# Kernel optimization log

Measured on AMD Instinct MI355X. Metric: run time of the kernel, lower is better.

## Reference

```python
import jax, jax.numpy as jnp
import numpy as np

# ---- DNC configuration (mirrors access_config / controller_config / args) ----
T, B, IN, OUT = 64, 32, 64, 64          # time, batch, input_size, output_size
N, Wd, R, NW = 128, 64, 4, 1            # memory_size, word_size, num_reads, num_writes
H = 256                                  # controller hidden_size (2 LSTM layers)
CLIP = 20.0
EPS = 1e-6
NUM_MODES = 2 * NW + 1                   # backward modes, forward modes, content mode
IF_SIZES = [R*Wd, R, NW*Wd, NW, NW*Wd, NW*Wd, R, NW, NW, R*NUM_MODES]
IF_SIZE = int(np.sum(IF_SIZES))


def setup_inputs() -> dict:
    key = jax.random.key(0)
    ks = jax.random.split(key, 12)
    in0 = IN + R * Wd  # controller input = external input + flattened prev reads

    def w(k, shape, fan):
        return jax.random.normal(k, shape, jnp.float32) / np.float32(np.sqrt(fan))

    return {
        "inputs": jax.random.normal(ks[0], (T, B, IN), jnp.float32),
        "Wx0": w(ks[1], (in0, 4 * H), in0),
        "Wh0": w(ks[2], (H, 4 * H), H),
        "b0": jnp.zeros((4 * H,), jnp.float32),
        "Wx1": w(ks[3], (H, 4 * H), H),
        "Wh1": w(ks[4], (H, 4 * H), H),
        "b1": jnp.zeros((4 * H,), jnp.float32),
        "W_if": w(ks[5], (H, IF_SIZE), H),
        "b_if": jnp.zeros((IF_SIZE,), jnp.float32),
        "W_out": w(ks[6], (H + R * Wd, OUT), H + R * Wd),
        "b_out": jnp.zeros((OUT,), jnp.float32),
    }


def _lstm(x, h, c, Wx, Wh, b):
    g = x @ Wx + h @ Wh + b
    i, f, gg, o = jnp.split(g, 4, axis=-1)
    c2 = jax.nn.sigmoid(f) * c + jax.nn.sigmoid(i) * jnp.tanh(gg)
    h2 = jax.nn.sigmoid(o) * jnp.tanh(c2)
    return h2, c2


def _content_weights(memory, keys, strengths):
    # memory [B,N,W], keys [B,h,W], strengths [B,h] -> [B,h,N]
    mnorm = jnp.linalg.norm(memory, axis=-1)          # [B,N]
    knorm = jnp.linalg.norm(keys, axis=-1)            # [B,h]
    dot = jnp.einsum('bhw,bnw->bhn', keys, memory)
    sim = dot / (knorm[..., None] * mnorm[:, None, :] + EPS)
    return jax.nn.softmax(sim * strengths[..., None], axis=-1)


def _allocation(usage):
    # usage [B,N] -> allocation weighting [B,N] (DNC freeness-based)
    usage = EPS + (1.0 - EPS) * usage
    order = jnp.argsort(usage, axis=-1)               # ascending usage (most free first)
    sorted_usage = jnp.take_along_axis(usage, order, axis=-1)
    prod = jnp.cumprod(sorted_usage, axis=-1)
    prod_excl = jnp.concatenate([jnp.ones_like(prod[:, :1]), prod[:, :-1]], axis=-1)
    alloc_sorted = (1.0 - sorted_usage) * prod_excl
    inv = jnp.argsort(order, axis=-1)
    return jnp.take_along_axis(alloc_sorted, inv, axis=-1)


def _dnc_forward(inputs, Wx0, Wh0, b0, Wx1, Wh1, b1, W_if, b_if, W_out, b_out):
    eye = 1.0 - jnp.eye(N, dtype=jnp.float32)
    splits = np.cumsum(IF_SIZES)[:-1]

    def step(state, x_t):
        h0, c0, h1, c1, M, rw, ww, link, prec, usage, reads = state
        ctrl_in = jnp.concatenate([x_t, reads.reshape(B, R * Wd)], axis=-1)
        h0, c0 = _lstm(ctrl_in, h0, c0, Wx0, Wh0, b0)
        h1, c1 = _lstm(h0, h1, c1, Wx1, Wh1, b1)
        ctrl = jnp.clip(h1, -CLIP, CLIP)

        p = jnp.split(ctrl @ W_if + b_if, splits, axis=-1)
        read_keys = p[0].reshape(B, R, Wd)
        read_str = 1.0 + jax.nn.softplus(p[1])              # oneplus
        write_keys = p[2].reshape(B, NW, Wd)
        write_str = 1.0 + jax.nn.softplus(p[3])
        erase = jax.nn.sigmoid(p[4]).reshape(B, NW, Wd)
        write_vec = p[5].reshape(B, NW, Wd)
        free_g = jax.nn.sigmoid(p[6])                       # [B,R]
        alloc_g = jax.nn.sigmoid(p[7])                      # [B,NW]
        write_g = jax.nn.sigmoid(p[8])                      # [B,NW]
        modes = jax.nn.softmax(p[9].reshape(B, R, NUM_MODES), axis=-1)

        # -- usage update (prev write weights, then free gates on prev reads) --
        cw = 1.0 - jnp.prod(1.0 - ww, axis=1)               # [B,N]
        u = usage + (1.0 - usage) * cw
        psi = jnp.prod(1.0 - free_g[..., None] * rw, axis=1)
        usage = u * psi

        # -- write weights: content + allocation, gated --
        wc = _content_weights(M, write_keys, write_str)     # [B,NW,N]
        u_tmp = usage
        ww_heads = []
        for i in range(NW):
            a = _allocation(u_tmp)
            wg = write_g[:, i:i+1]
            ag = alloc_g[:, i:i+1]
            ww_heads.append(wg * (ag * a + (1.0 - ag) * wc[:, i]))
            u_tmp = u_tmp + (1.0 - u_tmp) * wg * a
        ww = jnp.stack(ww_heads, axis=1)                    # [B,NW,N]

        # -- erase + write memory --
        erase_m = jnp.prod(1.0 - ww[..., None] * erase[:, :, None, :], axis=1)  # [B,N,W]
        add_m = jnp.einsum('bwn,bwk->bnk', ww, write_vec)
        M = M * erase_m + add_m

        # -- temporal link matrix + precedence --
        wi = ww[..., :, None]
        wj = ww[..., None, :]
        link = ((1.0 - wi - wj) * link + wi * prec[..., None, :]) * eye
        prec = (1.0 - ww.sum(axis=-1, keepdims=True)) * prec + ww

        # -- read weights: backward / content / forward modes --
        rc = _content_weights(M, read_keys, read_str)       # [B,R,N]
        fwd = jnp.einsum('bwij,brj->brwi', link, rw)
        bwd = jnp.einsum('bwji,brj->brwi', link, rw)
        bmode = modes[..., :NW]
        fmode = modes[..., NW:2*NW]
        cmode = modes[..., 2*NW]
        rw = (jnp.einsum('brw,brwn->brn', bmode, bwd)
              + cmode[..., None] * rc
              + jnp.einsum('brw,brwn->brn', fmode, fwd))
        reads = jnp.einsum('brn,bnk->brk', rw, M)           # [B,R,W]

        out = jnp.clip(jnp.concatenate([ctrl, reads.reshape(B, R * Wd)], axis=-1) @ W_out + b_out,
                       -CLIP, CLIP)
        return (h0, c0, h1, c1, M, rw, ww, link, prec, usage, reads), out

    z = jnp.zeros
    init = (z((B, H)), z((B, H)), z((B, H)), z((B, H)),
            z((B, N, Wd)), z((B, R, N)), z((B, NW, N)),
            z((B, NW, N, N)), z((B, NW, N)), z((B, N)), z((B, R, Wd)))
    _, outs = jax.lax.scan(step, init, inputs)
    return outs                                            # [T,B,OUT]


def reference(inputs, Wx0, Wh0, b0, Wx1, Wh1, b1, W_if, b_if, W_out, b_out):
    return _dnc_forward(inputs, Wx0, Wh0, b0, Wx1, Wh1, b1, W_if, b_if, W_out, b_out)
```

## Files before the change

kernel.cpp:

```cpp
#include <hip/hip_runtime.h>
#include <math.h>


#define TT   64
#define BB   32
#define INW  64
#define OUTW 64
#define NN   128
#define WD   64
#define RR   4
#define HH   256
#define IFSZ 471
#define CLIPV 20.0f
#define EPSV  1e-6f
#define NBLK 96

#define OFF_RK   0
#define OFF_RSTR 256
#define OFF_WK   260
#define OFF_WSTR 324
#define OFF_ER   325
#define OFF_WV   389
#define OFF_FG   453
#define OFF_AG   457
#define OFF_WG   458
#define OFF_MD   459

#define S_WSTR 0
#define S_AG   1
#define S_WG   2
#define S_KNW  3
#define S_RSTR 8
#define S_FG   12
#define S_KNR  16
#define S_BM   20
#define S_FM   24
#define S_CM   28

#define A_XS   0
#define A_GL   11840
#define A_C0   12896
#define A_GO   13152
#define A_WS   13216
#define A_WO   34528
#define B_XS   0
#define B_GL   9472
#define B_C1   10528
#define B_W1   10784
#define C_MS   0
#define C_LS   8320
#define C_WW   24832
#define C_PRC  24960
#define C_USG  25088
#define C_RWS  25216
#define C_IFC  25728
#define C_FWD  26208
#define C_BWD  26720
#define C_U2   27232
#define C_WCS  27360
#define C_RCS  27488
#define C_MNO  28000
#define C_ERS  28384
#define C_WVS  28448
#define C_SC   28512
#define C_SCAL 28576
#define C_PART2 28608

#define SMEM_FLOATS 36064
#define SMEM_BYTES  (SMEM_FLOATS*4)

#define W_CTL  0
#define W_RDS  8192
#define W_H0   16384
#define W_H1   32768
#define W_FLA  49152
#define W_FLB  (W_FLA + 1024)
#define W_FLC  (W_FLB + 1024)
#define W_END  (W_FLC + 1024)

__device__ __forceinline__ float sigf(float x){ return 1.0f/(1.0f+expf(-x)); }
__device__ __forceinline__ float sofp(float x){ return fmaxf(x,0.0f)+log1pf(expf(-fabsf(x))); }

__device__ __forceinline__ float gload(const float* p){
  return __hip_atomic_load(p, __ATOMIC_RELAXED, __HIP_MEMORY_SCOPE_AGENT);
}
__device__ __forceinline__ void gstore(float* p, float v){
  __hip_atomic_store(p, v, __ATOMIC_RELAXED, __HIP_MEMORY_SCOPE_AGENT);
}
__device__ __forceinline__ void gload8(const float* p, float* a, float* b){
  union { unsigned long long u; float f[2]; } w;
  w.u = __hip_atomic_load((const unsigned long long*)p,
                          __ATOMIC_RELAXED, __HIP_MEMORY_SCOPE_AGENT);
  *a = w.f[0]; *b = w.f[1];
}
__device__ __forceinline__ void gstore8(float* p, float a, float b){
  union { unsigned long long u; float f[2]; } w;
  w.f[0]=a; w.f[1]=b;
  __hip_atomic_store((unsigned long long*)p, w.u,
                     __ATOMIC_RELAXED, __HIP_MEMORY_SCOPE_AGENT);
}

__device__ __forceinline__ void waitflag(const unsigned* slots, unsigned target){
  if (threadIdx.x < 64){
    for (;;){
      unsigned m = __hip_atomic_load(&slots[(threadIdx.x & 31)*32],
                                     __ATOMIC_RELAXED, __HIP_MEMORY_SCOPE_AGENT);
      #pragma unroll
      for (int s=32;s>0;s>>=1){
        unsigned o = (unsigned)__shfl_xor((int)m, s, 64);
        m = (o < m) ? o : m;
      }
      if (m >= target) break;
      __builtin_amdgcn_s_sleep(2);
    }
  }
  __syncthreads();
}

__device__ __forceinline__ void setflag(unsigned* slots, int g, unsigned val){
  asm volatile("s_waitcnt vmcnt(0)" ::: "memory");
  __syncthreads();
  if (threadIdx.x == 0)
    __hip_atomic_store(&slots[g*32], val, __ATOMIC_RELAXED, __HIP_MEMORY_SCOPE_AGENT);
}

__device__ __forceinline__ float wredSum(float v){
  #pragma unroll
  for (int m=32;m>0;m>>=1) v += __shfl_xor(v,m,64);
  return v;
}
__device__ __forceinline__ float wredMax(float v){
  #pragma unroll
  for (int m=32;m>0;m>>=1) v = fmaxf(v,__shfl_xor(v,m,64));
  return v;
}

__device__ __forceinline__ float bfly64(float (&A)[64], int l, int* jb){
  #pragma unroll
  for (int st=0; st<6; ++st){
    const int m = 1<<st, half = 32>>st;
    const bool hi = (l & m) != 0;
    #pragma unroll
    for (int j=0;j<half;j++){
      float a = A[j], b = A[j+half];
      float keep = hi? b : a;
      float send = hi? a : b;
      A[j] = keep + __shfl_xor(send, m, 64);
    }
  }
  *jb = ((l&1)?32:0)|((l&2)?16:0)|((l&4)?8:0)|((l&8)?4:0)|((l&16)?2:0)|((l&32)?1:0);
  return A[0];
}

#define TILE_FMA(WBASE, WROW, XROW)                                      \
  {                                                                      \
    float xv[8], wv[8];                                                  \
    _Pragma("unroll")                                                    \
    for (int q=0;q<8;q++){                                               \
      wv[q] = sm[(WBASE) + (WROW)*37 + c0 + q];                          \
      xv[q] = Xs[(XROW)*37 + b0 + q];                                    \
    }                                                                    \
    _Pragma("unroll")                                                    \
    for (int bi=0;bi<8;bi++)                                             \
      _Pragma("unroll")                                                  \
      for (int ci=0;ci<8;ci++)                                           \
        acc[bi*8+ci] += xv[bi]*wv[ci];                                   \
  }

extern "C" __global__ __launch_bounds__(1024, 1)
void dnc_coop13(const float* __restrict__ inputs,
                const float* __restrict__ Wx0, const float* __restrict__ Wh0, const float* __restrict__ b0g,
                const float* __restrict__ Wx1, const float* __restrict__ Wh1, const float* __restrict__ b1g,
                const float* __restrict__ Wifg, const float* __restrict__ bifg,
                const float* __restrict__ Woutg, const float* __restrict__ boutg,
                float* __restrict__ outg, float* __restrict__ ws)
{
  const int bid  = blockIdx.x;
  const int role = bid >> 5;
  const int g    = bid & 31;
  const int tid  = threadIdx.x;
  const int lane = tid & 63;
  const int wid  = tid >> 6;

  extern __shared__ float sm[];

  float* gctl  = ws + W_CTL;
  float* greads= ws + W_RDS;
  unsigned* fA = (unsigned*)(ws + W_FLA);
  unsigned* fB = (unsigned*)(ws + W_FLB);
  unsigned* fC = (unsigned*)(ws + W_FLC);

  if (role == 0){
    for (int i = tid; i < 576*32; i += 1024){
      int r = i >> 5, cl = i & 31;
      int cglob = 8*g + (cl&7) + ((cl>>3)<<8);
      float v;
      if (r < 256)      v = Wx0[(64+r)*1024 + cglob];
      else if (r < 320) v = Wx0[(r-256)*1024 + cglob];
      else              v = Wh0[(r-320)*1024 + cglob];
      sm[A_WS + r*37 + cl] = v;
    }
    for (int i = tid; i < 512*2; i += 1024){
      int k = i >> 1, c = i & 1;
      sm[A_WO + k*3 + c] = Woutg[k*64 + 2*g + c];
    }
    if (tid < 256) sm[A_C0 + tid] = 0.0f;
  } else if (role == 1){
    for (int i = tid; i < 512*32; i += 1024){
      int r = i >> 5, cl = i & 31;
      int cglob = 8*g + (cl&7) + ((cl>>3)<<8);
      sm[B_W1 + r*37 + cl] = (r < 256) ? Wx1[r*1024 + cglob]
                                       : Wh1[(r-256)*1024 + cglob];
    }
    if (tid < 256) sm[B_C1 + tid] = 0.0f;
  } else {
    for (int i = tid; i < NN*65;  i += 1024) sm[C_MS + i] = 0.0f;
    for (int i = tid; i < NN*129; i += 1024) sm[C_LS + i] = 0.0f;
    if (tid < 128){ sm[C_WW+tid]=0.f; sm[C_PRC+tid]=0.f; sm[C_USG+tid]=0.f; }
    if (tid < 512) sm[C_RWS+tid]=0.f;
  }
  __syncthreads();

  if (role == 0){
    float* Xs = sm + A_XS;
    for (int t = 0; t <= TT; ++t){
      float* h0old = ws + W_H0 + (t&1)*8192;
      float* h0new = ws + W_H0 + ((t+1)&1)*8192;
      float acc[64]; float accO[16];

      waitflag(fA, (unsigned)t);
      if (t < TT){
        for (int i = tid; i < 256*16; i += 1024){
          int k = i>>4, b2 = (i&15)*2;
          float x0,x1; gload8(&h0old[k*32+b2], &x0,&x1);
          Xs[k*37+b2]=x0; Xs[k*37+b2+1]=x1;
        }
        for (int i = tid; i < 64*32; i += 1024){
          int bb = i>>6, k = i&63;
          Xs[(256+k)*37+bb] = inputs[(t*BB + bb)*INW + k];
        }
        __syncthreads();
        #pragma unroll
        for (int j=0;j<64;j++) acc[j]=0.f;
        {
          const int b0 = (wid>>2)*8, c0 = (wid&3)*8;
          #pragma unroll
          for (int i=0;i<4;i++){
            int k = i*64 + lane;
            TILE_FMA(A_WS, 320+k, k)
          }
          TILE_FMA(A_WS, 256+lane, 256+lane)
        }
        __syncthreads();
      }
      if (t > 0){
        waitflag(fB, (unsigned)t);
        for (int i = tid; i < 256*16; i += 1024){
          int k = i>>4, b2 = (i&15)*2;
          float x0,x1; gload8(&gctl[k*32+b2], &x0,&x1);
          Xs[k*37+b2]=x0; Xs[k*37+b2+1]=x1;
        }
        __syncthreads();
        #pragma unroll
        for (int j=0;j<16;j++) accO[j]=0.f;
        if (wid < 4){
          const int b0 = wid*8;
          #pragma unroll
          for (int i=0;i<4;i++){
            int k = i*64 + lane;
            float w0 = sm[A_WO + k*3], w1 = sm[A_WO + k*3 + 1];
            float xv[8];
            #pragma unroll
            for (int q=0;q<8;q++) xv[q] = Xs[k*37 + b0 + q];
            #pragma unroll
            for (int bi=0;bi<8;bi++){
              accO[bi*2]   += xv[bi]*w0;
              accO[bi*2+1] += xv[bi]*w1;
            }
          }
        }
        __syncthreads();
      }
      waitflag(fC, (unsigned)t);
      for (int i = tid; i < 32*128; i += 1024){
        int b = i>>7, k2 = (i&127)*2;
        float x0,x1; gload8(&greads[b*256+k2], &x0,&x1);
        Xs[k2*37+b]=x0; Xs[(k2+1)*37+b]=x1;
      }
      __syncthreads();
      if (t < TT){
        {
          const int b0 = (wid>>2)*8, c0 = (wid&3)*8;
          #pragma unroll
          for (int i=0;i<4;i++){
            int k = i*64 + lane;
            TILE_FMA(A_WS, k, k)
          }
          int jb; float v = bfly64(acc, lane, &jb);
          sm[A_GL + (b0 + (jb>>3))*33 + c0 + (jb&7)] = v;
        }
        __syncthreads();
        if (tid < 128){
          int t2 = tid*2, j = t2>>5, bb = t2&31;
          float hv[2];
          #pragma unroll
          for (int q=0;q<2;q++){
            int b_ = bb+q;
            float gi = sm[A_GL + b_*33 + j]      + b0g[8*g + j];
            float gf = sm[A_GL + b_*33 + 8 + j]  + b0g[256 + 8*g + j];
            float gg = sm[A_GL + b_*33 + 16 + j] + b0g[512 + 8*g + j];
            float go = sm[A_GL + b_*33 + 24 + j] + b0g[768 + 8*g + j];
            float c = sigf(gf)*sm[A_C0 + j*32 + b_] + sigf(gi)*tanhf(gg);
            sm[A_C0 + j*32 + b_] = c;
            hv[q] = sigf(go)*tanhf(c);
          }
          gstore8(&h0new[256*g + t2], hv[0], hv[1]);
        }
        setflag(fA, g, (unsigned)(t+1));
      }
      if (t > 0){
        if (wid < 4){
          const int b0 = wid*8;
          #pragma unroll
          for (int i=0;i<4;i++){
            int k = i*64 + lane;
            float w0 = sm[A_WO + (256+k)*3], w1 = sm[A_WO + (256+k)*3 + 1];
            float xv[8];
            #pragma unroll
            for (int q=0;q<8;q++) xv[q] = Xs[k*37 + b0 + q];
            #pragma unroll
            for (int bi=0;bi<8;bi++){
              accO[bi*2]   += xv[bi]*w0;
              accO[bi*2+1] += xv[bi]*w1;
            }
          }
          #pragma unroll
          for (int st=0; st<4; ++st){
            const int m = 1<<st, half = 8>>st;
            const bool hi = (lane & m) != 0;
            #pragma unroll
            for (int j=0;j<half;j++){
              float a = accO[j], b = accO[j+half];
              float keep = hi? b : a;
              float send = hi? a : b;
              accO[j] = keep + __shfl_xor(send, m, 64);
            }
          }
          accO[0] += __shfl_xor(accO[0], 16, 64);
          accO[0] += __shfl_xor(accO[0], 32, 64);
          int jb = ((lane&1)?8:0)|((lane&2)?4:0)|((lane&4)?2:0)|((lane&8)?1:0);
          if ((lane & 48) == 0){
            int bi = jb>>1, ci = jb&1;
            sm[A_GO + (wid*8+bi)*2 + ci] = accO[0];
          }
        }
        __syncthreads();
        if (tid < 64){
          int bb = tid>>1, c = tid&1;
          float v = sm[A_GO + tid] + boutg[2*g + c];
          outg[((t-1)*BB + bb)*OUTW + 2*g + c] = fminf(CLIPV, fmaxf(-CLIPV, v));
        }
      }
    }
  } else if (role == 1){
    float* Xs = sm + B_XS;
    for (int t = 0; t < TT; ++t){
      float* h0new = ws + W_H0 + ((t+1)&1)*8192;
      float* h1old = ws + W_H1 + (t&1)*8192;
      float* h1new = ws + W_H1 + ((t+1)&1)*8192;
      float acc[64];
      #pragma unroll
      for (int j=0;j<64;j++) acc[j]=0.f;

      waitflag(fB, (unsigned)t);
      for (int i = tid; i < 256*16; i += 1024){
        int k = i>>4, b2 = (i&15)*2;
        float x0,x1; gload8(&h1old[k*32+b2], &x0,&x1);
        Xs[k*37+b2]=x0; Xs[k*37+b2+1]=x1;
      }
      __syncthreads();
      {
        const int b0 = (wid>>2)*8, c0 = (wid&3)*8;
        #pragma unroll
        for (int i=0;i<4;i++){
          int k = i*64 + lane;
          TILE_FMA(B_W1, 256+k, k)
        }
      }
      __syncthreads();
      waitflag(fA, (unsigned)(t+1));
      for (int i = tid; i < 256*16; i += 1024){
        int k = i>>4, b2 = (i&15)*2;
        float x0,x1; gload8(&h0new[k*32+b2], &x0,&x1);
        Xs[k*37+b2]=x0; Xs[k*37+b2+1]=x1;
      }
      __syncthreads();
      {
        const int b0 = (wid>>2)*8, c0 = (wid&3)*8;
        #pragma unroll
        for (int i=0;i<4;i++){
          int k = i*64 + lane;
          TILE_FMA(B_W1, k, k)
        }
        int jb; float v = bfly64(acc, lane, &jb);
        sm[B_GL + (b0 + (jb>>3))*33 + c0 + (jb&7)] = v;
      }
      __syncthreads();
      if (tid < 128){
        int t2 = tid*2, j = t2>>5, bb = t2&31;
        float hv[2], cl2[2];
        #pragma unroll
        for (int q=0;q<2;q++){
          int b_ = bb+q;
          float gi = sm[B_GL + b_*33 + j]      + b1g[8*g + j];
          float gf = sm[B_GL + b_*33 + 8 + j]  + b1g[256 + 8*g + j];
          float gg = sm[B_GL + b_*33 + 16 + j] + b1g[512 + 8*g + j];
          float go = sm[B_GL + b_*33 + 24 + j] + b1g[768 + 8*g + j];
          float c = sigf(gf)*sm[B_C1 + j*32 + b_] + sigf(gi)*tanhf(gg);
          sm[B_C1 + j*32 + b_] = c;
          float h = sigf(go)*tanhf(c);
          hv[q] = h;
          cl2[q] = fminf(CLIPV, fmaxf(-CLIPV, h));
        }
        gstore8(&h1new[256*g + t2], hv[0], hv[1]);
        gstore8(&gctl[256*g + t2], cl2[0], cl2[1]);
      }
      setflag(fB, g, (unsigned)(t+1));
    }
  } else {
    float* Ms  = sm + C_MS;
    float* Ls  = sm + C_LS;
    float* wws = sm + C_WW;
    float* prc = sm + C_PRC;
    float* usg = sm + C_USG;
    float* rws = sm + C_RWS;
    float* ifcl= sm + C_IFC;
    float* fwds= sm + C_FWD;
    float* bwds= sm + C_BWD;
    float* u2  = sm + C_U2;
    float* wcs = sm + C_WCS;
    float* rcs = sm + C_RCS;
    float* mno = sm + C_MNO;
    float* ers = sm + C_ERS;
    float* wvs = sm + C_WVS;
    float* sc  = sm + C_SC;
    float* scal= sm + C_SCAL;
    float* ctl_l = sm + C_RCS;
    float* part2 = sm + C_PART2;

    for (int t = 0; t < TT; ++t){
      if (tid < 128){
        float s=0.f;
        #pragma unroll 8
        for (int d=0;d<WD;d++){ float v=Ms[tid*65+d]; s+=v*v; }
        mno[tid]=sqrtf(s);
      }
      waitflag(fB, (unsigned)(t+1));
      if (tid < 256) ctl_l[tid] = gload(&gctl[tid*32 + g]);
      __syncthreads();
      {
        const int kq = tid >> 8, c = tid & 255;
        const int c2 = c + 256;
        const bool has2 = (c2 < IFSZ);
        const float* Wp = Wifg + (size_t)(kq*64)*IFSZ;
        const float* xp = ctl_l + kq*64;
        float a0=0.f, a1=0.f;
        #pragma unroll 8
        for (int k=0;k<64;k++){
          float x = xp[k];
          a0 += x * Wp[(size_t)k*IFSZ + c];
          if (has2) a1 += x * Wp[(size_t)k*IFSZ + c2];
        }
        part2[kq*512 + c] = a0;
        if (has2) part2[kq*512 + c2] = a1;
      }
      __syncthreads();
      if (tid < IFSZ)
        ifcl[tid] = part2[tid] + part2[512+tid] + part2[1024+tid] + part2[1536+tid] + bifg[tid];
      __syncthreads();

      if (tid < RR){
        scal[S_RSTR+tid]=1.0f+sofp(ifcl[OFF_RSTR+tid]);
        scal[S_FG+tid]  =sigf(ifcl[OFF_FG+tid]);
        float m0=ifcl[OFF_MD+tid*3], m1=ifcl[OFF_MD+tid*3+1], m2=ifcl[OFF_MD+tid*3+2];
        float mx=fmaxf(m0,fmaxf(m1,m2));
        float e0=expf(m0-mx), e1=expf(m1-mx), e2=expf(m2-mx);
        float s=e0+e1+e2;
        scal[S_BM+tid]=e0/s; scal[S_FM+tid]=e1/s; scal[S_CM+tid]=e2/s;
      }
      if (tid == 4) scal[S_WSTR]=1.0f+sofp(ifcl[OFF_WSTR]);
      if (tid == 5) scal[S_AG]=sigf(ifcl[OFF_AG]);
      if (tid == 6) scal[S_WG]=sigf(ifcl[OFF_WG]);
      if (tid >= 64 && tid < 128){
        int d=tid-64;
        ers[d]=sigf(ifcl[OFF_ER+d]);
        wvs[d]=ifcl[OFF_WV+d];
      }
      if (wid == 8){
        float v=ifcl[OFF_WK+lane]; float s=wredSum(v*v);
        if (lane==0) scal[S_KNW]=sqrtf(s);
      }
      if (wid >= 10 && wid < 14){
        int r=wid-10; float v=ifcl[OFF_RK+r*WD+lane]; float s=wredSum(v*v);
        if (lane==0) scal[S_KNR+r]=sqrtf(s);
      }
      __syncthreads();

      if (tid < NN){
        float dot=0.f;
        #pragma unroll 8
        for (int d=0;d<WD;d++) dot += ifcl[OFF_WK+d]*Ms[tid*65+d];
        wcs[tid] = dot/(scal[S_KNW]*mno[tid]+EPSV)*scal[S_WSTR];
      } else if (tid < 256){
        int n = tid-128;
        float cw = wws[n];
        float u  = usg[n] + (1.0f-usg[n])*cw;
        float psi=1.0f;
        #pragma unroll
        for (int r=0;r<RR;r++) psi *= 1.0f - scal[S_FG+r]*rws[r*NN+n];
        float us = u*psi;
        usg[n]=us;
        u2[n] = EPSV + (1.0f-EPSV)*us;
      }
      __syncthreads();
      if (tid < NN){ float mx=wredMax(wcs[tid]); if(lane==0) sc[wid]=mx; }
      __syncthreads();
      if (tid < NN){
        float mx=fmaxf(sc[0],sc[1]);
        float e=expf(wcs[tid]-mx);
        wcs[tid]=e;
        float s=wredSum(e); if(lane==0) sc[2+wid]=s;
      }
      __syncthreads();
      if (tid < 256){
        int n = tid & 127, h = tid >> 7;
        float ui = u2[n]; float p = 1.0f;
        int j0 = h*64;
        for (int j=j0; j<j0+64; j++){
          float uj = u2[j];
          bool take = (uj<ui) || (uj==ui && j<n);
          p *= take ? uj : 1.0f;
        }
        part2[h*128 + n] = p;
      }
      __syncthreads();
      if (tid < NN){
        float wcsum = sc[2]+sc[3];
        float ui=u2[tid];
        float p = part2[tid]*part2[128+tid];
        float a = (1.0f-ui)*p;
        float wwn = scal[S_WG]*( scal[S_AG]*a + (1.0f-scal[S_AG])*(wcs[tid]/wcsum) );
        wws[tid]=wwn;
        float s=wredSum(wwn); if(lane==0) sc[4+wid]=s;
      }
      __syncthreads();
      #pragma unroll
      for (int i=0;i<8;i++){
        int el=tid+i*1024, n=el>>6, d=el&63;
        float w=wws[n];
        Ms[n*65+d] = Ms[n*65+d]*(1.0f - w*ers[d]) + w*wvs[d];
      }
      #pragma unroll
      for (int i=0;i<16;i++){
        int el=tid+i*1024, li=el>>7, lj=el&127;
        float v = (li==lj) ? 0.0f
                : (1.0f - wws[li] - wws[lj])*Ls[li*129+lj] + wws[li]*prc[lj];
        Ls[li*129+lj]=v;
      }
      __syncthreads();
      if (tid < 512){
        int r=tid>>7, n=tid&127;
        float dot=0.f, q=0.f;
        #pragma unroll 8
        for (int d=0;d<WD;d++){
          float m = Ms[n*65+d];
          dot += ifcl[OFF_RK+r*WD+d]*m;
          q   += m*m;
        }
        rcs[tid] = dot/(scal[S_KNR+r]*sqrtf(q)+EPSV)*scal[S_RSTR+r];
      } else {
        int idx=tid-512, r=idx>>7, i=idx&127;
        float f=0.f, bw=0.f;
        const float* rwr = rws + r*NN;
        #pragma unroll 4
        for (int j=0;j<NN;j++){
          float rv=rwr[j];
          f  += Ls[i*129+j]*rv;
          bw += Ls[j*129+i]*rv;
        }
        fwds[idx]=f; bwds[idx]=bw;
      }
      __syncthreads();
      if (tid < 512){ float mx=wredMax(rcs[tid]); if(lane==0) sc[8+wid]=mx; }
      __syncthreads();
      if (tid < 512){
        int r=tid>>7;
        float mx=fmaxf(sc[8+r*2],sc[9+r*2]);
        float e=expf(rcs[tid]-mx);
        rcs[tid]=e;
        float s=wredSum(e); if(lane==0) sc[16+wid]=s;
      }
      __syncthreads();
      if (tid < 512){
        int r=tid>>7;
        float rsum = sc[16+r*2]+sc[17+r*2];
        rws[tid] = scal[S_BM+r]*bwds[tid] + scal[S_CM+r]*(rcs[tid]/rsum) + scal[S_FM+r]*fwds[tid];
      } else if (tid < 640){
        int n = tid-512;
        float wsm = sc[4]+sc[5];
        prc[n] = (1.0f - wsm)*prc[n] + wws[n];
      }
      __syncthreads();
      {
        int kq=tid>>8, j=tid&255, r=j>>6, d=j&63;
        float s=0.f;
        const float* rwr = rws + r*NN + kq*32;
        const float* mp  = Ms + (kq*32)*65 + d;
        #pragma unroll 8
        for (int n=0;n<32;n++) s += rwr[n]*mp[n*65];
        part2[kq*256 + j] = s;
      }
      __syncthreads();
      if (tid < 128){
        int k2 = tid*2;
        float s0 = part2[k2]  +part2[256+k2]  +part2[512+k2]  +part2[768+k2];
        float s1 = part2[k2+1]+part2[256+k2+1]+part2[512+k2+1]+part2[768+k2+1];
        gstore8(&greads[g*256 + k2], s0, s1);
      }
      setflag(fC, g, (unsigned)(t+1));
    }
  }
}

extern "C" void kernel_launch(void* const* d_in, const int* in_sizes, int n_in,
                              void* d_out, int out_size, void* d_ws, size_t ws_size,
                              hipStream_t stream)
{
  const float* inputs=(const float*)d_in[0];
  const float* Wx0   =(const float*)d_in[1];
  const float* Wh0   =(const float*)d_in[2];
  const float* b0    =(const float*)d_in[3];
  const float* Wx1   =(const float*)d_in[4];
  const float* Wh1   =(const float*)d_in[5];
  const float* b1    =(const float*)d_in[6];
  const float* Wif   =(const float*)d_in[7];
  const float* bif   =(const float*)d_in[8];
  const float* Wout  =(const float*)d_in[9];
  const float* bout  =(const float*)d_in[10];
  float* out = (float*)d_out;
  float* ws  = (float*)d_ws;

  hipMemsetAsync(ws, 0, W_END * sizeof(float), stream);

  hipFuncSetAttribute((const void*)dnc_coop13,
                      hipFuncAttributeMaxDynamicSharedMemorySize, SMEM_BYTES);

  void* args[] = { (void*)&inputs, (void*)&Wx0, (void*)&Wh0, (void*)&b0,
                   (void*)&Wx1, (void*)&Wh1, (void*)&b1, (void*)&Wif,
                   (void*)&bif, (void*)&Wout, (void*)&bout, (void*)&out,
                   (void*)&ws };
  hipLaunchCooperativeKernel((void*)dnc_coop13, dim3(NBLK), dim3(1024),
                             args, SMEM_BYTES, stream);
}
```

Measured before the change: 2.894 ms.

## Overlap read-key interface GEMV with allocation phase and use per-slot flag waits

```diff
diff --git a/kernel.cpp b/kernel.cpp
--- a/kernel.cpp
+++ b/kernel.cpp
@@ -32,7 +32,6 @@
 #define S_KNW  3
 #define S_RSTR 8
 #define S_FG   12
-#define S_KNR  16
 #define S_BM   20
 #define S_FM   24
 #define S_CM   28
@@ -84,9 +83,6 @@
 __device__ __forceinline__ float gload(const float* p){
   return __hip_atomic_load(p, __ATOMIC_RELAXED, __HIP_MEMORY_SCOPE_AGENT);
 }
-__device__ __forceinline__ void gstore(float* p, float v){
-  __hip_atomic_store(p, v, __ATOMIC_RELAXED, __HIP_MEMORY_SCOPE_AGENT);
-}
 __device__ __forceinline__ void gload8(const float* p, float* a, float* b){
   union { unsigned long long u; float f[2]; } w;
   w.u = __hip_atomic_load((const unsigned long long*)p,
@@ -99,19 +95,21 @@
   __hip_atomic_store((unsigned long long*)p, w.u,
                      __ATOMIC_RELAXED, __HIP_MEMORY_SCOPE_AGENT);
 }
+__device__ __forceinline__ unsigned fload(const unsigned* p){
+  return __hip_atomic_load(p, __ATOMIC_RELAXED, __HIP_MEMORY_SCOPE_AGENT);
+}
 
 __device__ __forceinline__ void waitflag(const unsigned* slots, unsigned target){
   if (threadIdx.x < 64){
     for (;;){
-      unsigned m = __hip_atomic_load(&slots[(threadIdx.x & 31)*32],
-                                     __ATOMIC_RELAXED, __HIP_MEMORY_SCOPE_AGENT);
+      unsigned m = fload(&slots[(threadIdx.x & 31)*32]);
       #pragma unroll
       for (int s=32;s>0;s>>=1){
         unsigned o = (unsigned)__shfl_xor((int)m, s, 64);
         m = (o < m) ? o : m;
       }
       if (m >= target) break;
-      __builtin_amdgcn_s_sleep(2);
+      __builtin_amdgcn_s_sleep(1);
     }
   }
   __syncthreads();
@@ -167,8 +165,13 @@
         acc[bi*8+ci] += xv[bi]*wv[ci];                                   \
   }
 
+#define IF2_CHUNK(K0,K1)                                                 \
+  { _Pragma("unroll 4")                                                  \
+    for (int k=(K0); k<(K1); ++k)                                        \
+      ifAcc += p2x[k] * p2W[(size_t)k*IFSZ]; }
+
 extern "C" __global__ __launch_bounds__(1024, 1)
-void dnc_coop13(const float* __restrict__ inputs,
+void dnc_coop14(const float* __restrict__ inputs,
                 const float* __restrict__ Wx0, const float* __restrict__ Wh0, const float* __restrict__ b0g,
                 const float* __restrict__ Wx1, const float* __restrict__ Wh1, const float* __restrict__ b1g,
                 const float* __restrict__ Wifg, const float* __restrict__ bifg,
@@ -281,11 +284,19 @@
         }
         __syncthreads();
       }
-      waitflag(fC, (unsigned)t);
-      for (int i = tid; i < 32*128; i += 1024){
-        int b = i>>7, k2 = (i&127)*2;
-        float x0,x1; gload8(&greads[b*256+k2], &x0,&x1);
-        Xs[k2*37+b]=x0; Xs[(k2+1)*37+b]=x1;
+      {
+        const int p0 = wid*2;
+        #pragma unroll
+        for (int pp=0;pp<2;++pp){
+          int b = p0+pp;
+          const unsigned* slot = &fC[b*32];
+          while (fload(slot) < (unsigned)t) __builtin_amdgcn_s_sleep(1);
+          float x0,x1;
+          gload8(&greads[b*256 + 2*lane], &x0,&x1);
+          Xs[(2*lane)*37+b]=x0; Xs[(2*lane+1)*37+b]=x1;
+          gload8(&greads[b*256 + 128 + 2*lane], &x0,&x1);
+          Xs[(128+2*lane)*37+b]=x0; Xs[(129+2*lane)*37+b]=x1;
+        }
       }
       __syncthreads();
       if (t < TT){
@@ -388,11 +399,20 @@
         }
       }
       __syncthreads();
-      waitflag(fA, (unsigned)(t+1));
-      for (int i = tid; i < 256*16; i += 1024){
-        int k = i>>4, b2 = (i&15)*2;
-        float x0,x1; gload8(&h0new[k*32+b2], &x0,&x1);
-        Xs[k*37+b2]=x0; Xs[k*37+b2+1]=x1;
+      {
+        const int p0 = wid*2;
+        #pragma unroll
+        for (int pp=0;pp<2;++pp){
+          int gp = p0+pp;
+          const unsigned* slot = &fA[gp*32];
+          while (fload(slot) < (unsigned)(t+1)) __builtin_amdgcn_s_sleep(1);
+          int j = lane>>4, b2 = (lane&15)*2;
+          float x0,x1;
+          gload8(&h0new[256*gp + j*32 + b2], &x0,&x1);
+          Xs[(8*gp+j)*37+b2]=x0; Xs[(8*gp+j)*37+b2+1]=x1;
+          gload8(&h0new[256*gp + (j+4)*32 + b2], &x0,&x1);
+          Xs[(8*gp+j+4)*37+b2]=x0; Xs[(8*gp+j+4)*37+b2+1]=x1;
+        }
       }
       __syncthreads();
       {
@@ -448,6 +468,10 @@
     float* ctl_l = sm + C_RCS;
     float* part2 = sm + C_PART2;
 
+    const int p2idx = (tid >= 512) ? (tid - 512) : 0;
+    const int p2col = p2idx & 255;
+    const int p2kh  = p2idx >> 8;
+
     for (int t = 0; t < TT; ++t){
       if (tid < 128){
         float s=0.f;
@@ -460,23 +484,18 @@
       __syncthreads();
       {
         const int kq = tid >> 8, c = tid & 255;
-        const int c2 = c + 256;
-        const bool has2 = (c2 < IFSZ);
-        const float* Wp = Wifg + (size_t)(kq*64)*IFSZ;
-        const float* xp = ctl_l + kq*64;
-        float a0=0.f, a1=0.f;
-        #pragma unroll 8
-        for (int k=0;k<64;k++){
-          float x = xp[k];
-          a0 += x * Wp[(size_t)k*IFSZ + c];
-          if (has2) a1 += x * Wp[(size_t)k*IFSZ + c2];
-        }
-        part2[kq*512 + c] = a0;
-        if (has2) part2[kq*512 + c2] = a1;
-      }
-      __syncthreads();
-      if (tid < IFSZ)
-        ifcl[tid] = part2[tid] + part2[512+tid] + part2[1024+tid] + part2[1536+tid] + bifg[tid];
+        if (c < 215){
+          const float* Wp = Wifg + (size_t)(kq*64)*IFSZ + 256 + c;
+          const float* xp = ctl_l + kq*64;
+          float a0=0.f;
+          #pragma unroll 8
+          for (int k=0;k<64;k++) a0 += xp[k] * Wp[(size_t)k*IFSZ];
+          part2[kq*256 + c] = a0;
+        }
+      }
+      __syncthreads();
+      if (tid < 215)
+        ifcl[256+tid] = part2[tid] + part2[256+tid] + part2[512+tid] + part2[768+tid] + bifg[256+tid];
       __syncthreads();
 
       if (tid < RR){
@@ -500,11 +519,11 @@
         float v=ifcl[OFF_WK+lane]; float s=wredSum(v*v);
         if (lane==0) scal[S_KNW]=sqrtf(s);
       }
-      if (wid >= 10 && wid < 14){
-        int r=wid-10; float v=ifcl[OFF_RK+r*WD+lane]; float s=wredSum(v*v);
-        if (lane==0) scal[S_KNR+r]=sqrtf(s);
-      }
-      __syncthreads();
+      __syncthreads();
+
+      float ifAcc = 0.0f;
+      const float* p2W = Wifg + (size_t)(p2kh*128)*IFSZ + p2col;
+      const float* p2x = ctl_l + p2kh*128;
 
       if (tid < NN){
         float dot=0.f;
@@ -521,16 +540,19 @@
         float us = u*psi;
         usg[n]=us;
         u2[n] = EPSV + (1.0f-EPSV)*us;
+      } else if (tid >= 512){
+        IF2_CHUNK(0,26)
       }
       __syncthreads();
       if (tid < NN){ float mx=wredMax(wcs[tid]); if(lane==0) sc[wid]=mx; }
+      else if (tid >= 512){ IF2_CHUNK(26,52) }
       __syncthreads();
       if (tid < NN){
         float mx=fmaxf(sc[0],sc[1]);
         float e=expf(wcs[tid]-mx);
         wcs[tid]=e;
         float s=wredSum(e); if(lane==0) sc[2+wid]=s;
-      }
+      } else if (tid >= 512){ IF2_CHUNK(52,78) }
       __syncthreads();
       if (tid < 256){
         int n = tid & 127, h = tid >> 7;
@@ -542,7 +564,7 @@
           p *= take ? uj : 1.0f;
         }
         part2[h*128 + n] = p;
-      }
+      } else if (tid >= 512){ IF2_CHUNK(78,103) }
       __syncthreads();
       if (tid < NN){
         float wcsum = sc[2]+sc[3];
@@ -552,8 +574,12 @@
         float wwn = scal[S_WG]*( scal[S_AG]*a + (1.0f-scal[S_AG])*(wcs[tid]/wcsum) );
         wws[tid]=wwn;
         float s=wredSum(wwn); if(lane==0) sc[4+wid]=s;
-      }
-      __syncthreads();
+      } else if (tid >= 512){
+        IF2_CHUNK(103,128)
+        part2[1024 + p2kh*256 + p2col] = ifAcc;
+      }
+      __syncthreads();
+      if (tid < 256) ifcl[tid] = part2[1024+tid] + part2[1280+tid] + bifg[tid];
       #pragma unroll
       for (int i=0;i<8;i++){
         int el=tid+i*1024, n=el>>6, d=el&63;
@@ -570,14 +596,16 @@
       __syncthreads();
       if (tid < 512){
         int r=tid>>7, n=tid&127;
-        float dot=0.f, q=0.f;
+        float dot=0.f, q=0.f, kn=0.f;
         #pragma unroll 8
         for (int d=0;d<WD;d++){
           float m = Ms[n*65+d];
-          dot += ifcl[OFF_RK+r*WD+d]*m;
+          float rk = ifcl[OFF_RK + r*WD + d];
+          dot += rk*m;
           q   += m*m;
-        }
-        rcs[tid] = dot/(scal[S_KNR+r]*sqrtf(q)+EPSV)*scal[S_RSTR+r];
+          kn  += rk*rk;
+        }
+        rcs[tid] = dot/(sqrtf(kn)*sqrtf(q)+EPSV)*scal[S_RSTR+r];
       } else {
         int idx=tid-512, r=idx>>7, i=idx&127;
         float f=0.f, bw=0.f;
@@ -652,13 +680,13 @@
 
   hipMemsetAsync(ws, 0, W_END * sizeof(float), stream);
 
-  hipFuncSetAttribute((const void*)dnc_coop13,
+  hipFuncSetAttribute((const void*)dnc_coop14,
                       hipFuncAttributeMaxDynamicSharedMemorySize, SMEM_BYTES);
 
   void* args[] = { (void*)&inputs, (void*)&Wx0, (void*)&Wh0, (void*)&b0,
                    (void*)&Wx1, (void*)&Wh1, (void*)&b1, (void*)&Wif,
                    (void*)&bif, (void*)&Wout, (void*)&bout, (void*)&out,
                    (void*)&ws };
-  hipLaunchCooperativeKernel((void*)dnc_coop13, dim3(NBLK), dim3(1024),
+  hipLaunchCooperativeKernel((void*)dnc_coop14, dim3(NBLK), dim3(1024),
                              args, SMEM_BYTES, stream);
 }
```

After: 3.215 ms. 11.1% more time.
